# Optimization experiments

Hardware: AMD Instinct MI355X
Metric: run time of the kernel (lower is better)

Reference implementation:

```python
import jax, jax.numpy as jnp
import numpy as np

DIM = 256
HID = DIM * 16

def setup_inputs() -> dict:
    key = jax.random.key(0)
    ks = jax.random.split(key, 6)
    B, L = 4, 2048
    x = jax.random.normal(ks[0], (B, L, DIM), dtype=jnp.float32)
    # nn.Linear(dim, hidden): weight [H, D], bias [H]
    WB = jax.random.normal(ks[1], (HID, DIM), dtype=jnp.float32) / np.sqrt(DIM)
    bB = jax.random.normal(ks[2], (HID,), dtype=jnp.float32) * 0.01
    # nn.Linear(hidden, dim): weight [D, H], bias [D]
    WC = jax.random.normal(ks[3], (DIM, HID), dtype=jnp.float32) / np.sqrt(HID)
    bC = jax.random.normal(ks[4], (DIM,), dtype=jnp.float32) * 0.01
    A = jax.random.normal(ks[5], (HID,), dtype=jnp.float32)
    return {"x": x, "WB": WB, "bB": bB, "WC": WC, "bC": bC, "A": A}

def reference(x, WB, bB, WC, bC, A):
    # b = B(x): [B, L, H]
    b = jnp.einsum('bld,hd->blh', x, WB) + bB
    a = jax.nn.sigmoid(A)  # [H], time-invariant decay
    # h_t = a * h_{t-1} + b_t  (h_0 from zero state) -> associative scan over L
    a_seq = jnp.broadcast_to(a, b.shape)
    def comb(c1, c2):
        a1, u1 = c1
        a2, u2 = c2
        return (a1 * a2, a2 * u1 + u2)
    _, h = jax.lax.associative_scan(comb, (a_seq, b), axis=1)  # [B, L, H]
    # C(h): [B, L, D]
    return jnp.einsum('blh,dh->bld', h, WC) + bC
```

## Files before the change

### kernel.cpp

```cpp
#include <hip/hip_runtime.h>
#include <hip/hip_bf16.h>

#define DIMSZ 256
#define HID 4096
#define BATCH 4
#define SEQ 2048
#define NCH 64
#define CLEN 32
#define SPLITK2 4
#define KCHUNK (HID / SPLITK2)
#define BM2 64

typedef __bf16 bf16_t;
typedef __bf16 bf16x8 __attribute__((ext_vector_type(8)));
typedef __bf16 bf16x4 __attribute__((ext_vector_type(4)));
typedef float  f32x4  __attribute__((ext_vector_type(4)));

__device__ __forceinline__ float sigmoidf_dev(float x) {
    return 1.0f / (1.0f + __expf(-x));
}

__device__ __forceinline__ void load_lds16(const bf16_t* g, bf16_t* l) {
    __builtin_amdgcn_global_load_lds(
        (const __attribute__((address_space(1))) void*)g,
        (__attribute__((address_space(3))) void*)l,
        16, 0, 0);
}

__global__ void cvt_all_kernel(const float* __restrict__ x,
                               const float* __restrict__ WB,
                               const float* __restrict__ WC,
                               bf16_t* __restrict__ xb,
                               bf16_t* __restrict__ WBb,
                               bf16_t* __restrict__ WCb) {
    int i = blockIdx.x * blockDim.x + threadIdx.x;
    const float* src; bf16_t* dst; int j;
    if (i < 524288)      { src = x;  dst = xb;  j = i; }
    else if (i < 786432) { src = WB; dst = WBb; j = i - 524288; }
    else                 { src = WC; dst = WCb; j = i - 786432; }
    float4 v = ((const float4*)src)[j];
    bf16x4 o;
    o[0] = (bf16_t)v.x; o[1] = (bf16_t)v.y;
    o[2] = (bf16_t)v.z; o[3] = (bf16_t)v.w;
    ((bf16x4*)dst)[j] = o;
}

__global__ void w2_swizzle_kernel(const bf16_t* __restrict__ WCb,
                                  bf16_t* __restrict__ Wt) {
    int id = blockIdx.x * blockDim.x + threadIdx.x;
    int lane = id & 63, g = (id >> 6) & 15, ks = id >> 10;
    int n = g * 16 + (lane & 15);
    int k = ks * 32 + (lane >> 4) * 8;
    *(bf16x8*)&Wt[(size_t)id * 8] = *(const bf16x8*)&WCb[(size_t)n * HID + k];
}

__global__ __launch_bounds__(256)
void gemm1_fused(const bf16_t* __restrict__ Ag, const bf16_t* __restrict__ Bg,
                 const float* __restrict__ bias, const float* __restrict__ Adecay,
                 bf16_t* __restrict__ Cg, float* __restrict__ totals)
{
    constexpr int K = DIMSZ, N = HID;
    constexpr int LDTILE = 136;
    __shared__ bf16_t As[128 * 32];
    __shared__ bf16_t Bs[128 * 32];
    __shared__ bf16_t tile[128 * LDTILE];

    const int tid = threadIdx.x, wave = tid >> 6, lane = tid & 63;
    const int wm = wave >> 1, wn = wave & 1, q = lane >> 4, r16 = lane & 15;
    const int mBase = blockIdx.x * 128, nBase = blockIdx.y * 128;
    const int srow = lane >> 2, scol = (lane & 3) << 3;

    f32x4 acc[4][4] = {};

    for (int k0 = 0; k0 < K; k0 += 32) {
        #pragma unroll
        for (int i = 0; i < 2; i++) {
            int c = wave * 2 + i;
            load_lds16(&Ag[(size_t)(mBase + c * 16 + srow) * K + k0 + scol], &As[c * 512]);
            load_lds16(&Bg[(size_t)(nBase + c * 16 + srow) * K + k0 + scol], &Bs[c * 512]);
        }
        __syncthreads();

        bf16x8 af[4], bfr[4];
        #pragma unroll
        for (int mt = 0; mt < 4; mt++)
            af[mt] = *(const bf16x8*)&As[(wm * 64 + mt * 16 + r16) * 32 + q * 8];
        #pragma unroll
        for (int nt = 0; nt < 4; nt++)
            bfr[nt] = *(const bf16x8*)&Bs[(wn * 64 + nt * 16 + r16) * 32 + q * 8];

        #pragma unroll
        for (int mt = 0; mt < 4; mt++)
            #pragma unroll
            for (int nt = 0; nt < 4; nt++)
                acc[mt][nt] = __builtin_amdgcn_mfma_f32_16x16x32_bf16(
                    af[mt], bfr[nt], acc[mt][nt], 0, 0, 0);
        __syncthreads();
    }

    #pragma unroll
    for (int nt = 0; nt < 4; nt++) {
        const int chl = wn * 64 + nt * 16 + r16;
        const float bv = bias[nBase + chl];
        #pragma unroll
        for (int mt = 0; mt < 4; mt++) {
            const int t0 = wm * 64 + mt * 16 + q * 4;
            #pragma unroll
            for (int rg = 0; rg < 4; rg++)
                tile[(t0 + rg) * LDTILE + chl] = (bf16_t)(acc[mt][nt][rg] + bv);
        }
    }
    __syncthreads();

    #pragma unroll
    for (int p = 0; p < 8; p++) {
        const int t = p * 16 + (tid >> 4);
        const int ch8 = (tid & 15) << 3;
        *(bf16x8*)&Cg[(size_t)(mBase + t) * N + nBase + ch8] =
            *(const bf16x8*)&tile[t * LDTILE + ch8];
    }

    #pragma unroll
    for (int t = 0; t < 2; t++) {
        int task = tid + t * 256;
        int ch = task & 127, ck = task >> 7;
        float a = sigmoidf_dev(Adecay[nBase + ch]);
        float tot = 0.f;
        #pragma unroll 8
        for (int i = 0; i < CLEN; i++)
            tot = a * tot + (float)tile[(ck * CLEN + i) * LDTILE + ch];
        int batch = mBase >> 11;
        int cg = ((mBase & 2047) >> 5) + ck;
        totals[(size_t)(batch * NCH + cg) * HID + nBase + ch] = tot;
    }
}

__global__ void scan_carries_kernel(const float* __restrict__ totals,
                                    const float* __restrict__ Adecay,
                                    float* __restrict__ carries)
{
    int gid = blockIdx.x * 64 + threadIdx.x;
    int ch    = gid & (HID - 1);
    int batch = gid >> 12;
    float a = sigmoidf_dev(Adecay[ch]);
    float aC = a;
    #pragma unroll
    for (int i = 0; i < 5; i++) aC *= aC;
    float carry = 0.f;
    #pragma unroll 8
    for (int c = 0; c < NCH; c++) {
        size_t idx = (size_t)(batch * NCH + c) * HID + ch;
        carries[idx] = carry;
        carry = aC * carry + totals[idx];
    }
}

__global__ __launch_bounds__(256)
void gemm2_fused(const bf16_t* __restrict__ bv, const bf16_t* __restrict__ Wt,
                 const float* __restrict__ Adecay, const float* __restrict__ carries,
                 float* __restrict__ P)
{
    constexpr int N = DIMSZ;
    constexpr int CKSTRIDE = BM2 * 32 + 32;
    __shared__ bf16_t hs[8 * CKSTRIDE];

    const int tid = threadIdx.x, wave = tid >> 6, lane = tid & 63;
    const int q = lane >> 4, r16 = lane & 15;
    const int mBase = blockIdx.x * BM2;
    const int kBase = blockIdx.y * KCHUNK;
    const int batch = mBase >> 11;
    const int chunk0 = (mBase & 2047) >> 5;

    f32x4 acc[4][4] = {};

    for (int s = 0; s < KCHUNK / 256; s++) {
        const int chSlab = kBase + s * 256;

        if (s > 0) __syncthreads();

        #pragma unroll
        for (int i = 0; i < 8; i++) {
            int ck = wave * 2 + (i >> 2);
            int g  = i & 3;
            load_lds16(&bv[(size_t)(mBase + g * 16 + (lane >> 2)) * HID
                           + chSlab + ck * 32 + ((lane & 3) << 3)],
                       &hs[ck * CKSTRIDE + g * 512]);
        }
        __syncthreads();

        {
            const int ck = tid >> 5, ch = tid & 31;
            const int c = chSlab + ck * 32 + ch;
            const float a = sigmoidf_dev(Adecay[c]);
            float st = carries[(size_t)(batch * NCH + chunk0) * HID + c];
            bf16_t* hp = &hs[ck * CKSTRIDE + ch];
            #pragma unroll 8
            for (int t = 0; t < BM2; t++) {
                st = a * st + (float)hp[t * 32];
                hp[t * 32] = (bf16_t)st;
            }
        }
        __syncthreads();

        const int ksBase = (kBase >> 5) + s * 8;
        #pragma unroll 2
        for (int ck = 0; ck < 8; ck++) {
            bf16x8 af[4], bfr[4];
            #pragma unroll
            for (int nt = 0; nt < 4; nt++)
                bfr[nt] = *(const bf16x8*)&Wt[
                    (((size_t)(ksBase + ck) * 16 + wave * 4 + nt) * 64 + lane) * 8];
            #pragma unroll
            for (int mt = 0; mt < 4; mt++)
                af[mt] = *(const bf16x8*)&hs[ck * CKSTRIDE + (mt * 16 + r16) * 32 + q * 8];
            #pragma unroll
            for (int mt = 0; mt < 4; mt++)
                #pragma unroll
                for (int nt = 0; nt < 4; nt++)
                    acc[mt][nt] = __builtin_amdgcn_mfma_f32_16x16x32_bf16(
                        af[mt], bfr[nt], acc[mt][nt], 0, 0, 0);
        }
    }

    float* Pb = P + (size_t)blockIdx.y * (BATCH * SEQ) * N;
    #pragma unroll
    for (int nt = 0; nt < 4; nt++) {
        const int col = wave * 64 + nt * 16 + r16;
        #pragma unroll
        for (int mt = 0; mt < 4; mt++) {
            const int row0 = mBase + mt * 16 + q * 4;
            #pragma unroll
            for (int rg = 0; rg < 4; rg++)
                Pb[(size_t)(row0 + rg) * N + col] = acc[mt][nt][rg];
        }
    }
}

__global__ void reduce_out_kernel(const float* __restrict__ P,
                                  const float* __restrict__ bias,
                                  float* __restrict__ out, int MN4) {
    int i = blockIdx.x * blockDim.x + threadIdx.x;
    if (i >= MN4) return;
    int n4 = i & (DIMSZ / 4 - 1);
    float4 acc = ((const float4*)bias)[n4];
    #pragma unroll
    for (int s = 0; s < SPLITK2; s++) {
        float4 p = ((const float4*)P)[(size_t)s * MN4 + i];
        acc.x += p.x; acc.y += p.y; acc.z += p.z; acc.w += p.w;
    }
    ((float4*)out)[i] = acc;
}

extern "C" void kernel_launch(void* const* d_in, const int* in_sizes, int n_in,
                              void* d_out, int out_size, void* d_ws, size_t ws_size,
                              hipStream_t stream)
{
    const float* x  = (const float*)d_in[0];
    const float* WB = (const float*)d_in[1];
    const float* bB = (const float*)d_in[2];
    const float* WC = (const float*)d_in[3];
    const float* bC = (const float*)d_in[4];
    const float* A  = (const float*)d_in[5];

    char* ws = (char*)d_ws;
    size_t off = 0;
    bf16_t* xb   = (bf16_t*)(ws + off); off += (size_t)BATCH * SEQ * DIMSZ * 2;
    bf16_t* WBb  = (bf16_t*)(ws + off); off += (size_t)HID * DIMSZ * 2;
    bf16_t* WCb  = (bf16_t*)(ws + off); off += (size_t)DIMSZ * HID * 2;
    bf16_t* Wt   = (bf16_t*)(ws + off); off += (size_t)DIMSZ * HID * 2;
    bf16_t* bbuf = (bf16_t*)(ws + off); off += (size_t)BATCH * SEQ * HID * 2;
    float* partials = (float*)(ws + off); off += (size_t)SPLITK2 * BATCH * SEQ * DIMSZ * 4;
    float* totals   = (float*)(ws + off); off += (size_t)BATCH * NCH * HID * 4;
    float* carries  = (float*)(ws + off); off += (size_t)BATCH * NCH * HID * 4;

    const int M = BATCH * SEQ;

    cvt_all_kernel<<<4096, 256, 0, stream>>>(x, WB, WC, xb, WBb, WCb);
    w2_swizzle_kernel<<<512, 256, 0, stream>>>(WCb, Wt);

    dim3 g1(M / 128, HID / 128);
    gemm1_fused<<<g1, 256, 0, stream>>>(xb, WBb, bB, A, bbuf, totals);

    scan_carries_kernel<<<256, 64, 0, stream>>>(totals, A, carries);

    dim3 g2(M / BM2, SPLITK2);
    gemm2_fused<<<g2, 256, 0, stream>>>(bbuf, Wt, A, carries, partials);
    reduce_out_kernel<<<(M * DIMSZ / 4 + 255) / 256, 256, 0, stream>>>(
        partials, bC, (float*)d_out, M * DIMSZ / 4);
}
```

Baseline: 158.9 us.

## Pre-swizzle GEMM1 operands into MFMA fragment layout and merge prep kernels

A single prep kernel now converts x, WB and WC to bf16 and writes each directly in the per-lane MFMA fragment order. This replaces the separate convert and swizzle kernels. GEMM1 then loads its fragments straight from global memory with coalesced 16-byte loads, with no LDS staging and no __syncthreads in the K loop. The aim is to remove a launch, one intermediate bf16 pass over WC, and the LDS and barrier overhead in GEMM1. The cost is that fragments are re-read from global/L2 by every block, without LDS reuse shared across waves.

```diff
diff --git a/kernel.cpp b/kernel.cpp
--- a/kernel.cpp
+++ b/kernel.cpp
@@ -13,7 +13,6 @@
 
 typedef __bf16 bf16_t;
 typedef __bf16 bf16x8 __attribute__((ext_vector_type(8)));
-typedef __bf16 bf16x4 __attribute__((ext_vector_type(4)));
 typedef float  f32x4  __attribute__((ext_vector_type(4)));
 
 __device__ __forceinline__ float sigmoidf_dev(float x) {
@@ -27,75 +26,72 @@
         16, 0, 0);
 }
 
-__global__ void cvt_all_kernel(const float* __restrict__ x,
-                               const float* __restrict__ WB,
-                               const float* __restrict__ WC,
-                               bf16_t* __restrict__ xb,
-                               bf16_t* __restrict__ WBb,
-                               bf16_t* __restrict__ WCb) {
+__device__ __forceinline__ bf16x8 cvt8(const float* p) {
+    bf16x8 o;
+    #pragma unroll
+    for (int j = 0; j < 8; j++) o[j] = (bf16_t)p[j];
+    return o;
+}
+
+__global__ void prep_kernel(const float* __restrict__ x,
+                            const float* __restrict__ WB,
+                            const float* __restrict__ WC,
+                            bf16_t* __restrict__ xt,
+                            bf16_t* __restrict__ WBt,
+                            bf16_t* __restrict__ Wt) {
     int i = blockIdx.x * blockDim.x + threadIdx.x;
-    const float* src; bf16_t* dst; int j;
-    if (i < 524288)      { src = x;  dst = xb;  j = i; }
-    else if (i < 786432) { src = WB; dst = WBb; j = i - 524288; }
-    else                 { src = WC; dst = WCb; j = i - 786432; }
-    float4 v = ((const float4*)src)[j];
-    bf16x4 o;
-    o[0] = (bf16_t)v.x; o[1] = (bf16_t)v.y;
-    o[2] = (bf16_t)v.z; o[3] = (bf16_t)v.w;
-    ((bf16x4*)dst)[j] = o;
-}
-
-__global__ void w2_swizzle_kernel(const bf16_t* __restrict__ WCb,
-                                  bf16_t* __restrict__ Wt) {
-    int id = blockIdx.x * blockDim.x + threadIdx.x;
-    int lane = id & 63, g = (id >> 6) & 15, ks = id >> 10;
-    int n = g * 16 + (lane & 15);
-    int k = ks * 32 + (lane >> 4) * 8;
-    *(bf16x8*)&Wt[(size_t)id * 8] = *(const bf16x8*)&WCb[(size_t)n * HID + k];
+    if (i < 262144) {
+        int lane = i & 63, m16 = (i >> 6) & 511, ks = i >> 15;
+        int row = m16 * 16 + (lane & 15);
+        int k   = ks * 32 + (lane >> 4) * 8;
+        *(bf16x8*)&xt[(size_t)i * 8] = cvt8(&x[(size_t)row * DIMSZ + k]);
+    } else if (i < 393216) {
+        int j = i - 262144;
+        int lane = j & 63, n16 = (j >> 6) & 255, ks = j >> 14;
+        int row = n16 * 16 + (lane & 15);
+        int k   = ks * 32 + (lane >> 4) * 8;
+        *(bf16x8*)&WBt[(size_t)j * 8] = cvt8(&WB[(size_t)row * DIMSZ + k]);
+    } else {
+        int j = i - 393216;
+        int lane = j & 63, g = (j >> 6) & 15, ks = j >> 10;
+        int row = g * 16 + (lane & 15);
+        int k   = ks * 32 + (lane >> 4) * 8;
+        *(bf16x8*)&Wt[(size_t)j * 8] = cvt8(&WC[(size_t)row * HID + k]);
+    }
 }
 
 __global__ __launch_bounds__(256)
-void gemm1_fused(const bf16_t* __restrict__ Ag, const bf16_t* __restrict__ Bg,
+void gemm1_fused(const bf16_t* __restrict__ xt, const bf16_t* __restrict__ WBt,
                  const float* __restrict__ bias, const float* __restrict__ Adecay,
                  bf16_t* __restrict__ Cg, float* __restrict__ totals)
 {
-    constexpr int K = DIMSZ, N = HID;
+    constexpr int N = HID;
     constexpr int LDTILE = 136;
-    __shared__ bf16_t As[128 * 32];
-    __shared__ bf16_t Bs[128 * 32];
     __shared__ bf16_t tile[128 * LDTILE];
 
     const int tid = threadIdx.x, wave = tid >> 6, lane = tid & 63;
     const int wm = wave >> 1, wn = wave & 1, q = lane >> 4, r16 = lane & 15;
     const int mBase = blockIdx.x * 128, nBase = blockIdx.y * 128;
-    const int srow = lane >> 2, scol = (lane & 3) << 3;
+    const int m16Base = blockIdx.x * 8 + wm * 4;
+    const int n16Base = blockIdx.y * 8 + wn * 4;
 
     f32x4 acc[4][4] = {};
 
-    for (int k0 = 0; k0 < K; k0 += 32) {
-        #pragma unroll
-        for (int i = 0; i < 2; i++) {
-            int c = wave * 2 + i;
-            load_lds16(&Ag[(size_t)(mBase + c * 16 + srow) * K + k0 + scol], &As[c * 512]);
-            load_lds16(&Bg[(size_t)(nBase + c * 16 + srow) * K + k0 + scol], &Bs[c * 512]);
-        }
-        __syncthreads();
-
+    #pragma unroll 2
+    for (int ks = 0; ks < 8; ks++) {
         bf16x8 af[4], bfr[4];
         #pragma unroll
         for (int mt = 0; mt < 4; mt++)
-            af[mt] = *(const bf16x8*)&As[(wm * 64 + mt * 16 + r16) * 32 + q * 8];
+            af[mt] = *(const bf16x8*)&xt[(((size_t)ks * 512 + m16Base + mt) * 64 + lane) * 8];
         #pragma unroll
         for (int nt = 0; nt < 4; nt++)
-            bfr[nt] = *(const bf16x8*)&Bs[(wn * 64 + nt * 16 + r16) * 32 + q * 8];
-
+            bfr[nt] = *(const bf16x8*)&WBt[(((size_t)ks * 256 + n16Base + nt) * 64 + lane) * 8];
         #pragma unroll
         for (int mt = 0; mt < 4; mt++)
             #pragma unroll
             for (int nt = 0; nt < 4; nt++)
                 acc[mt][nt] = __builtin_amdgcn_mfma_f32_16x16x32_bf16(
                     af[mt], bfr[nt], acc[mt][nt], 0, 0, 0);
-        __syncthreads();
     }
 
     #pragma unroll
@@ -264,9 +260,8 @@
 
     char* ws = (char*)d_ws;
     size_t off = 0;
-    bf16_t* xb   = (bf16_t*)(ws + off); off += (size_t)BATCH * SEQ * DIMSZ * 2;
-    bf16_t* WBb  = (bf16_t*)(ws + off); off += (size_t)HID * DIMSZ * 2;
-    bf16_t* WCb  = (bf16_t*)(ws + off); off += (size_t)DIMSZ * HID * 2;
+    bf16_t* xt   = (bf16_t*)(ws + off); off += (size_t)BATCH * SEQ * DIMSZ * 2;
+    bf16_t* WBt  = (bf16_t*)(ws + off); off += (size_t)HID * DIMSZ * 2;
     bf16_t* Wt   = (bf16_t*)(ws + off); off += (size_t)DIMSZ * HID * 2;
     bf16_t* bbuf = (bf16_t*)(ws + off); off += (size_t)BATCH * SEQ * HID * 2;
     float* partials = (float*)(ws + off); off += (size_t)SPLITK2 * BATCH * SEQ * DIMSZ * 4;
@@ -275,11 +270,10 @@
 
     const int M = BATCH * SEQ;
 
-    cvt_all_kernel<<<4096, 256, 0, stream>>>(x, WB, WC, xb, WBb, WCb);
-    w2_swizzle_kernel<<<512, 256, 0, stream>>>(WCb, Wt);
+    prep_kernel<<<2048, 256, 0, stream>>>(x, WB, WC, xt, WBt, Wt);
 
     dim3 g1(M / 128, HID / 128);
-    gemm1_fused<<<g1, 256, 0, stream>>>(xb, WBb, bB, A, bbuf, totals);
+    gemm1_fused<<<g1, 256, 0, stream>>>(xt, WBt, bB, A, bbuf, totals);
 
     scan_carries_kernel<<<256, 64, 0, stream>>>(totals, A, carries);
 
```

New measurement: 153.6 us. 1.04x faster.
